# Optimization experiments

Measured on AMD Instinct MI355X. Metric: run time of the kernel, lower is better.

## Reference

```python
import jax, jax.numpy as jnp
import numpy as np

D_MODEL, N_LEVELS, N_HEADS, N_POINTS = 256, 4, 8, 4
SHAPES = [(100, 100), (50, 50), (25, 25), (13, 13)]  # (H, W) per level


def setup_inputs() -> dict:
    key = jax.random.key(0)
    ks = jax.random.split(key, 8)
    N = 2
    C = D_MODEL
    Len_in = sum(h * w for h, w in SHAPES)
    Lq = Len_in  # encoder self-attention
    query = jax.random.normal(ks[0], (N, Lq, C), jnp.float32)
    reference_points = jax.random.uniform(ks[1], (N, Lq, N_LEVELS, 2), dtype=jnp.float32)
    input_flatten = jax.random.normal(ks[2], (N, Len_in, C), jnp.float32)
    input_spatial_shapes = np.array(SHAPES, dtype=np.int64)
    areas = input_spatial_shapes[:, 0] * input_spatial_shapes[:, 1]
    input_level_start_index = np.concatenate([[0], np.cumsum(areas)[:-1]]).astype(np.int64)
    s = 1.0 / np.sqrt(C)
    Wv = jax.random.uniform(ks[3], (C, C), jnp.float32, -s, s)
    bv = jnp.zeros((C,), jnp.float32)
    # sampling_offsets: small random weight + the module's grid bias init
    Woff = jax.random.normal(ks[4], (N_HEADS * N_LEVELS * N_POINTS * 2, C), jnp.float32) * 0.01
    thetas = jnp.arange(N_HEADS, dtype=jnp.float32) * (2.0 * np.pi / N_HEADS)
    grid = jnp.stack([jnp.cos(thetas), jnp.sin(thetas)], -1)  # (M,2)
    grid = grid / jnp.max(jnp.abs(grid), axis=-1, keepdims=True)
    grid = jnp.tile(grid[:, None, None, :], (1, N_LEVELS, N_POINTS, 1))
    grid = grid * (jnp.arange(N_POINTS, dtype=jnp.float32) + 1.0)[None, None, :, None]
    boff = grid.reshape(-1)
    Wa = jax.random.normal(ks[5], (N_HEADS * N_LEVELS * N_POINTS, C), jnp.float32) * 0.02
    ba = jnp.zeros((N_HEADS * N_LEVELS * N_POINTS,), jnp.float32)
    Wo = jax.random.uniform(ks[6], (C, C), jnp.float32, -s, s)
    bo = jnp.zeros((C,), jnp.float32)
    return {
        'query': query, 'reference_points': reference_points, 'input_flatten': input_flatten,
        'input_spatial_shapes': input_spatial_shapes, 'input_level_start_index': input_level_start_index,
        'Wv': Wv, 'bv': bv, 'Woff': Woff, 'boff': boff, 'Wa': Wa, 'ba': ba, 'Wo': Wo, 'bo': bo,
    }


def _msda_forward(query, reference_points, input_flatten, shapes, starts,
                  Wv, bv, Woff, boff, Wa, ba, Wo, bo):
    N, Lq, C = query.shape
    M, L, P = N_HEADS, N_LEVELS, N_POINTS
    D = C // M
    value = (input_flatten @ Wv.T + bv).reshape(N, -1, M, D)  # (N, Len_in, M, D)
    off = (query @ Woff.T + boff).reshape(N, Lq, M, L, P, 2)
    attn = jax.nn.softmax((query @ Wa.T + ba).reshape(N, Lq, M, L * P), axis=-1)
    attn = attn.reshape(N, Lq, M, L, P)
    # offset_normalizer = (W_l, H_l)
    norm = jnp.asarray(shapes[:, ::-1].copy(), jnp.float32)  # (L, 2)
    loc = reference_points[:, :, None, :, None, :] + off / norm[None, None, None, :, None, :]
    grids = 2.0 * loc - 1.0  # (N, Lq, M, L, P, 2), grid_sample convention
    out = jnp.zeros((N, Lq, M, D), query.dtype)
    for l in range(L):
        H, W = int(shapes[l, 0]), int(shapes[l, 1])
        s0 = int(starts[l])
        v = value[:, s0:s0 + H * W]  # (N, H*W, M, D)
        # align_corners=False unnormalization
        gx = ((grids[:, :, :, l, :, 0] + 1.0) * W - 1.0) / 2.0  # (N, Lq, M, P)
        gy = ((grids[:, :, :, l, :, 1] + 1.0) * H - 1.0) / 2.0
        x0 = jnp.floor(gx); y0 = jnp.floor(gy)
        fx = gx - x0;       fy = gy - y0
        x0i = x0.astype(jnp.int32); y0i = y0.astype(jnp.int32)

        def gather(iy, ix):
            valid = (iy >= 0) & (iy < H) & (ix >= 0) & (ix < W)
            lin = jnp.clip(iy, 0, H - 1) * W + jnp.clip(ix, 0, W - 1)  # (N, Lq, M, P)
            lin2 = lin.transpose(0, 1, 3, 2).reshape(N, Lq * P, M)
            g = jnp.take_along_axis(v, lin2[..., None], axis=1)  # (N, Lq*P, M, D)
            g = g.reshape(N, Lq, P, M, D).transpose(0, 1, 3, 2, 4)  # (N, Lq, M, P, D)
            return g * valid[..., None]  # zero padding outside

        s00 = gather(y0i, x0i)
        s01 = gather(y0i, x0i + 1)
        s10 = gather(y0i + 1, x0i)
        s11 = gather(y0i + 1, x0i + 1)
        sampled = (s00 * ((1 - fy) * (1 - fx))[..., None] + s01 * ((1 - fy) * fx)[..., None]
                   + s10 * (fy * (1 - fx))[..., None] + s11 * (fy * fx)[..., None])
        out = out + jnp.einsum('nqmp,nqmpd->nqmd', attn[:, :, :, l], sampled)
    out = out.reshape(N, Lq, C)
    return out @ Wo.T + bo


def reference(query, reference_points, input_flatten, input_spatial_shapes, input_level_start_index,
              Wv, bv, Woff, boff, Wa, ba, Wo, bo):
    shapes = np.asarray(input_spatial_shapes)
    starts = np.asarray(input_level_start_index)
    return _msda_forward(query, reference_points, input_flatten, shapes, starts,
                         Wv, bv, Woff, boff, Wa, ba, Wo, bo)
```

## Files before the change

kernel.cpp:

```cpp
#include <hip/hip_runtime.h>
#include <math.h>

#define NB   2
#define LQ   13294
#define NROWS (NB*LQ)
#define CDIM 256
#define HSLICES (NROWS + 1)
#define HS32 ((size_t)HSLICES * 32)

typedef unsigned short u16;
typedef unsigned int   u32;
typedef short bf16x8 __attribute__((ext_vector_type(8)));
typedef float f32x4  __attribute__((ext_vector_type(4)));
typedef float f32x2  __attribute__((ext_vector_type(2)));

struct alignas(8) U16x4 { u16 x, y, z, w; };

__device__ __forceinline__ u16 f2bf(float f) {
    u32 u = __builtin_bit_cast(u32, f);
    u += 0x7FFFu + ((u >> 16) & 1u);
    return (u16)(u >> 16);
}

__device__ __forceinline__ void gload_lds16(const void* g, void* l) {
    __builtin_amdgcn_global_load_lds(
        (__attribute__((address_space(1))) void*)g,
        (__attribute__((address_space(3))) void*)l, 16, 0, 0);
}

__device__ __forceinline__ f32x2 bfpair(u32 u) {
    union { u32 w[2]; f32x2 v; } x;
    x.w[0] = u << 16;
    x.w[1] = u & 0xFFFF0000u;
    return x.v;
}

__global__ __launch_bounds__(256)
void prep_all(const float4* __restrict__ query, const float4* __restrict__ inflat,
              const float* __restrict__ Wv, const float* __restrict__ Woff,
              const float* __restrict__ Wa, const float* __restrict__ Wo,
              u16* __restrict__ qb, u16* __restrict__ ib,
              u16* __restrict__ wb) {
    const int b = blockIdx.x;
    const int t = threadIdx.x;
    if (b < 6647) {
        int i = b * 256 + t;
        float4 v = query[i];
        U16x4 o{f2bf(v.x), f2bf(v.y), f2bf(v.z), f2bf(v.w)};
        *(U16x4*)&qb[(size_t)i * 4] = o;
    } else if (b < 13294) {
        int i = (b - 6647) * 256 + t;
        float4 v = inflat[i];
        U16x4 o{f2bf(v.x), f2bf(v.y), f2bf(v.z), f2bf(v.w)};
        *(U16x4*)&ib[(size_t)i * 4] = o;
    } else {
        int i = (b - 13294) * 256 + t;
        float v;
        if      (i <  65536) v = Wv[i];
        else if (i < 131072) v = Woff[i - 65536];
        else if (i < 163840) v = Wa[i - 131072];
        else                 v = Wo[i - 163840];
        wb[i] = f2bf(v);
    }
}

__device__ __forceinline__ void gemm_core64(
    const u16* __restrict__ A, const u16* __restrict__ Bw, int M, int row0,
    u16* As, u16* Bs, f32x4 (&acc)[2][4]) {
    const int tid  = threadIdx.x;
    const int lane = tid & 63;
    const int wave = tid >> 6;
    const int ln16 = lane & 15;
    const int kq   = lane >> 4;
    const int wr   = (wave >> 1) * 32;
    const int wc   = (wave & 1) * 64;

    #pragma unroll
    for (int kt = 0; kt < 4; ++kt) {
        const int k0 = kt * 64;
        #pragma unroll
        for (int it = 0; it < 2; ++it) {
            int chunk = it * 256 + tid;
            int row = chunk >> 3, ch = chunk & 7;
            int chs = (ch ^ (row & 7)) * 8;
            int gra = min(row0 + row, M - 1);
            gload_lds16(A + (size_t)gra * 256 + k0 + chs, As + chunk * 8);
        }
        #pragma unroll
        for (int it = 0; it < 4; ++it) {
            int cb = it * 256 + tid;
            int row = cb >> 3, ch = cb & 7;
            int chs = (ch ^ (row & 7)) * 8;
            gload_lds16(Bw + (size_t)row * 256 + k0 + chs, Bs + cb * 8);
        }
        __syncthreads();
        #pragma unroll
        for (int kf = 0; kf < 2; ++kf) {
            const int ck = kf * 4 + kq;
            bf16x8 a[2], b[4];
            #pragma unroll
            for (int i = 0; i < 2; ++i) {
                int r = wr + i * 16 + ln16;
                a[i] = *(const bf16x8*)&As[r * 64 + ((ck ^ (r & 7)) * 8)];
            }
            #pragma unroll
            for (int j = 0; j < 4; ++j) {
                int c = wc + j * 16 + ln16;
                b[j] = *(const bf16x8*)&Bs[c * 64 + ((ck ^ (c & 7)) * 8)];
            }
            #pragma unroll
            for (int i = 0; i < 2; ++i)
                #pragma unroll
                for (int j = 0; j < 4; ++j)
                    acc[i][j] = __builtin_amdgcn_mfma_f32_16x16x32_bf16(
                        a[i], b[j], acc[i][j], 0, 0, 0);
        }
        __syncthreads();
    }
}

__global__ __launch_bounds__(256, 4)
void gemm_front(const u16* __restrict__ qb, const u16* __restrict__ ib,
                const u16* __restrict__ wb, const float* __restrict__ bv,
                const float* __restrict__ boff, const float* __restrict__ ba,
                u16* __restrict__ value, float* __restrict__ offb,
                float* __restrict__ logit, int M) {
    __shared__ u16 Sh[64 * 64 + 128 * 64];
    u16* As = Sh;
    u16* Bs = Sh + 4096;
    const int lid  = blockIdx.x;
    const int xcd  = lid & 7;
    const int idx  = lid >> 3;
    const int rg   = xcd * 52 + idx / 5;
    const int s    = idx % 5;
    const int row0 = rg * 64;
    const u16* A  = (s < 2) ? ib : qb;
    const u16* Bw = wb + (size_t)s * 32768;
    const float* bias = (s == 0) ? bv
                      : (s == 1) ? bv + 128
                      : (s == 2) ? boff
                      : (s == 3) ? boff + 128
                      : ba;

    f32x4 acc[2][4] = {};
    gemm_core64(A, Bw, M, row0, As, Bs, acc);

    const int tid  = threadIdx.x;
    const int lane = tid & 63;
    const int wave = tid >> 6;
    const int ln16 = lane & 15, kq = lane >> 4;
    const int wr = (wave >> 1) * 32, wc = (wave & 1) * 64;

    if (s < 2) {
        #pragma unroll
        for (int j = 0; j < 4; ++j) {
            int cl = wc + j * 16 + ln16;
            float bj = bias[cl];
            #pragma unroll
            for (int i = 0; i < 2; ++i)
                #pragma unroll
                for (int r = 0; r < 4; ++r) {
                    int rl = wr + i * 16 + kq * 4 + r;
                    Sh[rl * 128 + cl] = f2bf(acc[i][j][r] + bj);
                }
        }
        __syncthreads();
        #pragma unroll
        for (int it = 0; it < 4; ++it) {
            int ci = it * 256 + tid;
            int tr = ci >> 4;
            int cc = ci & 15;
            int gr = row0 + tr;
            if (gr < M) {
                int cg = s * 128 + cc * 8;
                u16* dst = value + (size_t)(cg >> 5) * HS32
                                 + (size_t)gr * 32 + (cg & 31);
                *(uint4*)dst = *(const uint4*)&Sh[tr * 128 + cc * 8];
            }
        }
        if (s == 0 && rg == 0) {
            value[(size_t)(tid >> 5) * HS32 + (size_t)NROWS * 32 + (tid & 31)] = 0;
        }
    } else {
        #pragma unroll
        for (int j = 0; j < 4; ++j) {
            int lc = wc + j * 16 + ln16;
            float bj = bias[lc];
            #pragma unroll
            for (int i = 0; i < 2; ++i) {
                #pragma unroll
                for (int r = 0; r < 4; ++r) {
                    int gr = row0 + wr + i * 16 + kq * 4 + r;
                    if (gr < M) {
                        float o = acc[i][j][r] + bj;
                        if (s < 4)
                            offb[(size_t)gr * 256 + (s - 2) * 128 + lc] = o;
                        else
                            logit[(size_t)gr * 128 + lc] = o;
                    }
                }
            }
        }
    }
}

__global__ __launch_bounds__(256, 4)
void gemm_out(const u16* __restrict__ A, const u16* __restrict__ Bw0,
              const float* __restrict__ bias, float* __restrict__ C, int M) {
    __shared__ u16 Sh[64 * 64 + 128 * 64];
    u16* As = Sh;
    u16* Bs = Sh + 4096;
    const int lid  = blockIdx.x;
    const int xcd  = lid & 7;
    const int idx  = lid >> 3;
    const int rg   = xcd * 52 + idx / 2;
    const int s    = idx % 2;
    const int row0 = rg * 64;
    const u16* Bw = Bw0 + (size_t)s * 32768;

    f32x4 acc[2][4] = {};
    gemm_core64(A, Bw, M, row0, As, Bs, acc);

    const int lane = threadIdx.x & 63;
    const int wave = threadIdx.x >> 6;
    const int ln16 = lane & 15, kq = lane >> 4;
    const int wr = (wave >> 1) * 32, wc = (wave & 1) * 64;
    #pragma unroll
    for (int j = 0; j < 4; ++j) {
        int gc = s * 128 + wc + j * 16 + ln16;
        float bj = bias[gc];
        #pragma unroll
        for (int i = 0; i < 2; ++i) {
            #pragma unroll
            for (int r = 0; r < 4; ++r) {
                int gr = row0 + wr + i * 16 + kq * 4 + r;
                if (gr < M) C[(size_t)gr * 256 + gc] = acc[i][j][r] + bj;
            }
        }
    }
}

__global__ __launch_bounds__(256, 4)
void msda_sample(const u16* __restrict__ value,
                 const float* __restrict__ refpts,
                 const float* __restrict__ off,
                 const float* __restrict__ logits,
                 u16* __restrict__ tmp) {
    __shared__ float sAw[4][8][16];
    __shared__ int   sLin[4][8][17][2];
    __shared__ float sW[4][8][17][4];

    const int t  = threadIdx.x;
    const int qb = blockIdx.x * 4;

    if (t < 32) {
        const int qi = t >> 3, m = t & 7;
        const float* lg = logits + (size_t)(qb + qi) * 128 + m * 16;
        float e[16];
        float mx = -1e30f;
        #pragma unroll
        for (int i = 0; i < 16; ++i) { e[i] = lg[i]; mx = fmaxf(mx, e[i]); }
        float s = 0.f;
        #pragma unroll
        for (int i = 0; i < 16; ++i) { e[i] = __expf(e[i] - mx); s += e[i]; }
        const float inv = 1.f / s;
        #pragma unroll
        for (int i = 0; i < 16; ++i) sAw[qi][m][i] = e[i] * inv;
    }
    __syncthreads();

    #pragma unroll
    for (int j2 = 0; j2 < 2; ++j2) {
        const int job = t + j2 * 256;
        const int qi = job >> 7;
        const int m  = (job >> 4) & 7;
        const int p  = job & 15;
        const int l  = p >> 2, pp = p & 3;
        const int q  = qb + qi;
        const int n  = (q >= LQ) ? 1 : 0;

        const int W = (l == 0) ? 100 : (l == 1) ? 50 : (l == 2) ? 25 : 13;
        const int H = W;
        const int st = (l == 0) ? 0 : (l == 1) ? 10000 : (l == 2) ? 12500 : 13125;
        const float invW = (l == 0) ? 0.01f : (l == 1) ? 0.02f
                         : (l == 2) ? 0.04f : (1.f / 13.f);

        const float rx = refpts[(size_t)q * 8 + l * 2 + 0];
        const float ry = refpts[(size_t)q * 8 + l * 2 + 1];
        const float ox = off[(size_t)q * 256 + m * 32 + (l * 4 + pp) * 2 + 0];
        const float oy = off[(size_t)q * 256 + m * 32 + (l * 4 + pp) * 2 + 1];

        const float locx = rx + ox * invW;
        const float locy = ry + oy * invW;
        const float grx = 2.f * locx - 1.f;
        const float gry = 2.f * locy - 1.f;
        const float gx = ((grx + 1.f) * (float)W - 1.f) * 0.5f;
        const float gy = ((gry + 1.f) * (float)H - 1.f) * 0.5f;
        const float x0f = floorf(gx), y0f = floorf(gy);
        const float fx = gx - x0f, fy = gy - y0f;
        const int x0 = (int)x0f, y0 = (int)y0f;
        const int x1 = x0 + 1, y1 = y0 + 1;

        const int cx0 = min(max(x0, 0), W - 1);
        const int cy0 = min(max(y0, 0), H - 1);
        const int cy1 = min(max(y1, 0), H - 1);
        const bool vx0 = (x0 >= 0) & (x0 < W);
        const bool vx1 = (x1 >= 0) & (x1 < W);
        const bool vy0 = (y0 >= 0) & (y0 < H);
        const bool vy1 = (y1 >= 0) & (y1 < H);

        const float aw = sAw[qi][m][p];
        const int base = n * LQ + st;
        const float w00 = (vy0 & vx0) ? aw * (1.f - fy) * (1.f - fx) : 0.f;
        const float w01 = (vy0 & vx1) ? aw * (1.f - fy) * fx         : 0.f;
        const float w10 = (vy1 & vx0) ? aw * fy * (1.f - fx)         : 0.f;
        const float w11 = (vy1 & vx1) ? aw * fy * fx                 : 0.f;
        const bool fold = (x0 < 0);
        sLin[qi][m][p][0] = base + cy0 * W + cx0;
        sLin[qi][m][p][1] = base + cy1 * W + cx0;
        sW[qi][m][p][0] = fold ? w01 : w00;
        sW[qi][m][p][1] = fold ? 0.f : w01;
        sW[qi][m][p][2] = fold ? w11 : w10;
        sW[qi][m][p][3] = fold ? 0.f : w11;
    }
    __syncthreads();

    const int qi = t >> 6;
    const int m  = (t >> 3) & 7;
    const int e  = t & 7;
    const int xh = e >> 2;
    const int c4 = e & 3;
    const int q  = qb + qi;
    const char* vb = (const char*)value + (size_t)m * (HS32 * 2);
    const u32 eoff = (u32)e * 16u;

    f32x2 a2[4] = {{0.f, 0.f}, {0.f, 0.f}, {0.f, 0.f}, {0.f, 0.f}};

    int2   rbA = *(const int2*)  &sLin[qi][m][0][0];
    float4 w4A = *(const float4*)&sW  [qi][m][0][0];
    uint4  rA0 = *(const uint4*)(vb + ((u32)rbA.x * 64u + eoff));
    uint4  rA1 = *(const uint4*)(vb + ((u32)rbA.y * 64u + eoff));

    #pragma unroll
    for (int p = 0; p < 16; ++p) {
        int2   rbB; float4 w4B; uint4 rB0, rB1;
        if (p < 15) {
            rbB = *(const int2*)  &sLin[qi][m][p + 1][0];
            w4B = *(const float4*)&sW  [qi][m][p + 1][0];
            rB0 = *(const uint4*)(vb + ((u32)rbB.x * 64u + eoff));
            rB1 = *(const uint4*)(vb + ((u32)rbB.y * 64u + eoff));
        } else {
            rbB = rbA; w4B = w4A; rB0 = rA0; rB1 = rA1;
        }
        const float wa  = xh ? w4A.y : w4A.x;
        const float wb_ = xh ? w4A.w : w4A.z;
        f32x2 wa2 = {wa, wa};
        f32x2 wb2 = {wb_, wb_};
        a2[0] += wa2 * bfpair(rA0.x); a2[1] += wa2 * bfpair(rA0.y);
        a2[2] += wa2 * bfpair(rA0.z); a2[3] += wa2 * bfpair(rA0.w);
        a2[0] += wb2 * bfpair(rA1.x); a2[1] += wb2 * bfpair(rA1.y);
        a2[2] += wb2 * bfpair(rA1.z); a2[3] += wb2 * bfpair(rA1.w);
        rbA = rbB; w4A = w4B; rA0 = rB0; rA1 = rB1;
    }
    #pragma unroll
    for (int k = 0; k < 4; ++k) {
        a2[k].x += __shfl_xor(a2[k].x, 4);
        a2[k].y += __shfl_xor(a2[k].y, 4);
    }
    if (xh == 0) {
        uint4 o;
        o.x = (u32)f2bf(a2[0].x) | ((u32)f2bf(a2[0].y) << 16);
        o.y = (u32)f2bf(a2[1].x) | ((u32)f2bf(a2[1].y) << 16);
        o.z = (u32)f2bf(a2[2].x) | ((u32)f2bf(a2[2].y) << 16);
        o.w = (u32)f2bf(a2[3].x) | ((u32)f2bf(a2[3].y) << 16);
        *(uint4*)((char*)tmp + ((u32)q * 512u + (u32)m * 64u + (u32)c4 * 16u)) = o;
    }
}

extern "C" void kernel_launch(void* const* d_in, const int* in_sizes, int n_in,
                              void* d_out, int out_size, void* d_ws, size_t ws_size,
                              hipStream_t stream) {
    const float* query  = (const float*)d_in[0];
    const float* refpts = (const float*)d_in[1];
    const float* inflat = (const float*)d_in[2];
    const float* Wv   = (const float*)d_in[5];
    const float* bv   = (const float*)d_in[6];
    const float* Woff = (const float*)d_in[7];
    const float* boff = (const float*)d_in[8];
    const float* Wa   = (const float*)d_in[9];
    const float* ba   = (const float*)d_in[10];
    const float* Wo   = (const float*)d_in[11];
    const float* bo   = (const float*)d_in[12];
    float* out = (float*)d_out;

    char* ws = (char*)d_ws;
    constexpr size_t SZ16  = (size_t)NROWS * 256 * 2;
    constexpr size_t SZVAL = ((size_t)HSLICES * 512 + 4095) & ~(size_t)4095;
    constexpr size_t SZ32  = (size_t)NROWS * 256 * 4;
    constexpr size_t SZL   = (size_t)NROWS * 128 * 4;
    u16*   qb    = (u16*)(ws);
    u16*   ib    = (u16*)(ws + SZ16);
    u16*   value = (u16*)(ws + 2 * SZ16);
    float* offb  = (float*)(ws + 2 * SZ16 + SZVAL);
    float* logit = (float*)(ws + 2 * SZ16 + SZVAL + SZ32);
    u16*   wb    = (u16*)(ws + 2 * SZ16 + SZVAL + SZ32 + SZL);
    u16*   tmp   = qb;

    hipLaunchKernelGGL(prep_all, dim3(14190), dim3(256), 0, stream,
                       (const float4*)query, (const float4*)inflat,
                       Wv, Woff, Wa, Wo, qb, ib, wb);

    gemm_front<<<dim3(2080), dim3(256), 0, stream>>>(
        qb, ib, wb, bv, boff, ba, value, offb, logit, NROWS);

    hipLaunchKernelGGL(msda_sample, dim3(NROWS / 4), dim3(256), 0, stream,
                       value, refpts, offb, logit, tmp);

    gemm_out<<<dim3(832), dim3(256), 0, stream>>>(
        tmp, wb + 163840, bo, out, NROWS);
}
```

Before: 199.7 us.

## Load GEMM MFMA operands directly from global memory, bypassing LDS staging

Replaces the LDS-staged GEMM core (global_load_lds with XOR swizzle and block barriers) with a version where each wave loads its bf16x8 MFMA fragments straight from global memory. This removes the barriers and LDS traffic, and gemm_out no longer needs shared memory, so more blocks may fit per CU. In exchange, operand tiles that several waves share are fetched redundantly through the caches. The 16-byte loads per lane along K are only partly coalesced, and the occupancy hint in launch_bounds is dropped.

```diff
diff --git a/kernel.cpp b/kernel.cpp
--- a/kernel.cpp
+++ b/kernel.cpp
@@ -20,12 +20,6 @@
     u32 u = __builtin_bit_cast(u32, f);
     u += 0x7FFFu + ((u >> 16) & 1u);
     return (u16)(u >> 16);
-}
-
-__device__ __forceinline__ void gload_lds16(const void* g, void* l) {
-    __builtin_amdgcn_global_load_lds(
-        (__attribute__((address_space(1))) void*)g,
-        (__attribute__((address_space(3))) void*)l, 16, 0, 0);
 }
 
 __device__ __forceinline__ f32x2 bfpair(u32 u) {
@@ -64,70 +58,52 @@
     }
 }
 
-__device__ __forceinline__ void gemm_core64(
+__device__ __forceinline__ void gemm_core_direct(
     const u16* __restrict__ A, const u16* __restrict__ Bw, int M, int row0,
-    u16* As, u16* Bs, f32x4 (&acc)[2][4]) {
-    const int tid  = threadIdx.x;
-    const int lane = tid & 63;
-    const int wave = tid >> 6;
+    f32x4 (&acc)[2][4]) {
+    const int lane = threadIdx.x & 63;
+    const int wave = threadIdx.x >> 6;
     const int ln16 = lane & 15;
     const int kq   = lane >> 4;
     const int wr   = (wave >> 1) * 32;
     const int wc   = (wave & 1) * 64;
 
-    #pragma unroll
-    for (int kt = 0; kt < 4; ++kt) {
-        const int k0 = kt * 64;
-        #pragma unroll
-        for (int it = 0; it < 2; ++it) {
-            int chunk = it * 256 + tid;
-            int row = chunk >> 3, ch = chunk & 7;
-            int chs = (ch ^ (row & 7)) * 8;
-            int gra = min(row0 + row, M - 1);
-            gload_lds16(A + (size_t)gra * 256 + k0 + chs, As + chunk * 8);
-        }
-        #pragma unroll
-        for (int it = 0; it < 4; ++it) {
-            int cb = it * 256 + tid;
-            int row = cb >> 3, ch = cb & 7;
-            int chs = (ch ^ (row & 7)) * 8;
-            gload_lds16(Bw + (size_t)row * 256 + k0 + chs, Bs + cb * 8);
-        }
-        __syncthreads();
-        #pragma unroll
-        for (int kf = 0; kf < 2; ++kf) {
-            const int ck = kf * 4 + kq;
-            bf16x8 a[2], b[4];
-            #pragma unroll
-            for (int i = 0; i < 2; ++i) {
-                int r = wr + i * 16 + ln16;
-                a[i] = *(const bf16x8*)&As[r * 64 + ((ck ^ (r & 7)) * 8)];
-            }
-            #pragma unroll
-            for (int j = 0; j < 4; ++j) {
-                int c = wc + j * 16 + ln16;
-                b[j] = *(const bf16x8*)&Bs[c * 64 + ((ck ^ (c & 7)) * 8)];
-            }
-            #pragma unroll
-            for (int i = 0; i < 2; ++i)
-                #pragma unroll
-                for (int j = 0; j < 4; ++j)
-                    acc[i][j] = __builtin_amdgcn_mfma_f32_16x16x32_bf16(
-                        a[i], b[j], acc[i][j], 0, 0, 0);
-        }
-        __syncthreads();
-    }
-}
-
-__global__ __launch_bounds__(256, 4)
+    const int ra0 = min(row0 + wr      + ln16, M - 1);
+    const int ra1 = min(row0 + wr + 16 + ln16, M - 1);
+    const u16* pa0 = A  + (size_t)ra0 * 256 + kq * 8;
+    const u16* pa1 = A  + (size_t)ra1 * 256 + kq * 8;
+    const u16* pb0 = Bw + (size_t)(wc      + ln16) * 256 + kq * 8;
+    const u16* pb1 = Bw + (size_t)(wc + 16 + ln16) * 256 + kq * 8;
+    const u16* pb2 = Bw + (size_t)(wc + 32 + ln16) * 256 + kq * 8;
+    const u16* pb3 = Bw + (size_t)(wc + 48 + ln16) * 256 + kq * 8;
+
+    #pragma unroll
+    for (int kf = 0; kf < 8; ++kf) {
+        const int ko = kf * 32;
+        bf16x8 a0 = *(const bf16x8*)(pa0 + ko);
+        bf16x8 a1 = *(const bf16x8*)(pa1 + ko);
+        bf16x8 b0 = *(const bf16x8*)(pb0 + ko);
+        bf16x8 b1 = *(const bf16x8*)(pb1 + ko);
+        bf16x8 b2 = *(const bf16x8*)(pb2 + ko);
+        bf16x8 b3 = *(const bf16x8*)(pb3 + ko);
+        acc[0][0] = __builtin_amdgcn_mfma_f32_16x16x32_bf16(a0, b0, acc[0][0], 0, 0, 0);
+        acc[0][1] = __builtin_amdgcn_mfma_f32_16x16x32_bf16(a0, b1, acc[0][1], 0, 0, 0);
+        acc[0][2] = __builtin_amdgcn_mfma_f32_16x16x32_bf16(a0, b2, acc[0][2], 0, 0, 0);
+        acc[0][3] = __builtin_amdgcn_mfma_f32_16x16x32_bf16(a0, b3, acc[0][3], 0, 0, 0);
+        acc[1][0] = __builtin_amdgcn_mfma_f32_16x16x32_bf16(a1, b0, acc[1][0], 0, 0, 0);
+        acc[1][1] = __builtin_amdgcn_mfma_f32_16x16x32_bf16(a1, b1, acc[1][1], 0, 0, 0);
+        acc[1][2] = __builtin_amdgcn_mfma_f32_16x16x32_bf16(a1, b2, acc[1][2], 0, 0, 0);
+        acc[1][3] = __builtin_amdgcn_mfma_f32_16x16x32_bf16(a1, b3, acc[1][3], 0, 0, 0);
+    }
+}
+
+__global__ __launch_bounds__(256)
 void gemm_front(const u16* __restrict__ qb, const u16* __restrict__ ib,
                 const u16* __restrict__ wb, const float* __restrict__ bv,
                 const float* __restrict__ boff, const float* __restrict__ ba,
                 u16* __restrict__ value, float* __restrict__ offb,
                 float* __restrict__ logit, int M) {
-    __shared__ u16 Sh[64 * 64 + 128 * 64];
-    u16* As = Sh;
-    u16* Bs = Sh + 4096;
+    __shared__ u16 Sh[64 * 128];
     const int lid  = blockIdx.x;
     const int xcd  = lid & 7;
     const int idx  = lid >> 3;
@@ -143,7 +119,7 @@
                       : ba;
 
     f32x4 acc[2][4] = {};
-    gemm_core64(A, Bw, M, row0, As, Bs, acc);
+    gemm_core_direct(A, Bw, M, row0, acc);
 
     const int tid  = threadIdx.x;
     const int lane = tid & 63;
@@ -204,12 +180,9 @@
     }
 }
 
-__global__ __launch_bounds__(256, 4)
+__global__ __launch_bounds__(256)
 void gemm_out(const u16* __restrict__ A, const u16* __restrict__ Bw0,
               const float* __restrict__ bias, float* __restrict__ C, int M) {
-    __shared__ u16 Sh[64 * 64 + 128 * 64];
-    u16* As = Sh;
-    u16* Bs = Sh + 4096;
     const int lid  = blockIdx.x;
     const int xcd  = lid & 7;
     const int idx  = lid >> 3;
@@ -219,7 +192,7 @@
     const u16* Bw = Bw0 + (size_t)s * 32768;
 
     f32x4 acc[2][4] = {};
-    gemm_core64(A, Bw, M, row0, As, Bs, acc);
+    gemm_core_direct(A, Bw, M, row0, acc);
 
     const int lane = threadIdx.x & 63;
     const int wave = threadIdx.x >> 6;
```

Result: slower. 255.1 us (+27.7%).

## Fuse fp32-to-bf16 activation conversion into front GEMM A-tile loads

Applied to the files above, without the earlier changes.

Removes the separate pass that converted query and input_flatten to bf16. The front GEMM now loads fp32 A tiles straight into LDS with a swizzle and converts them to bf16 in registers with v_cvt_pk_bf16_f32 before the MFMA. Only the small weight conversion remains as its own kernel. This saves a full read and write of both activations, but each A tile now moves twice as many bytes and takes twice the LDS, and the four weight-shard blocks per row group each re-read the fp32 rows.

```diff
diff --git a/kernel.cpp b/kernel.cpp
--- a/kernel.cpp
+++ b/kernel.cpp
@@ -22,6 +22,12 @@
     return (u16)(u >> 16);
 }
 
+__device__ __forceinline__ u32 cvtpk(float a, float b) {
+    u32 d;
+    asm("v_cvt_pk_bf16_f32 %0, %1, %2" : "=v"(d) : "v"(a), "v"(b));
+    return d;
+}
+
 __device__ __forceinline__ void gload_lds16(const void* g, void* l) {
     __builtin_amdgcn_global_load_lds(
         (__attribute__((address_space(1))) void*)g,
@@ -36,32 +42,16 @@
 }
 
 __global__ __launch_bounds__(256)
-void prep_all(const float4* __restrict__ query, const float4* __restrict__ inflat,
-              const float* __restrict__ Wv, const float* __restrict__ Woff,
-              const float* __restrict__ Wa, const float* __restrict__ Wo,
-              u16* __restrict__ qb, u16* __restrict__ ib,
-              u16* __restrict__ wb) {
-    const int b = blockIdx.x;
-    const int t = threadIdx.x;
-    if (b < 6647) {
-        int i = b * 256 + t;
-        float4 v = query[i];
-        U16x4 o{f2bf(v.x), f2bf(v.y), f2bf(v.z), f2bf(v.w)};
-        *(U16x4*)&qb[(size_t)i * 4] = o;
-    } else if (b < 13294) {
-        int i = (b - 6647) * 256 + t;
-        float4 v = inflat[i];
-        U16x4 o{f2bf(v.x), f2bf(v.y), f2bf(v.z), f2bf(v.w)};
-        *(U16x4*)&ib[(size_t)i * 4] = o;
-    } else {
-        int i = (b - 13294) * 256 + t;
-        float v;
-        if      (i <  65536) v = Wv[i];
-        else if (i < 131072) v = Woff[i - 65536];
-        else if (i < 163840) v = Wa[i - 131072];
-        else                 v = Wo[i - 163840];
-        wb[i] = f2bf(v);
-    }
+void prep_w(const float* __restrict__ Wv, const float* __restrict__ Woff,
+            const float* __restrict__ Wa, const float* __restrict__ Wo,
+            u16* __restrict__ wb) {
+    int i = blockIdx.x * 256 + threadIdx.x;
+    float v;
+    if      (i <  65536) v = Wv[i];
+    else if (i < 131072) v = Woff[i - 65536];
+    else if (i < 163840) v = Wa[i - 131072];
+    else                 v = Wo[i - 163840];
+    wb[i] = f2bf(v);
 }
 
 __device__ __forceinline__ void gemm_core64(
@@ -119,23 +109,84 @@
     }
 }
 
+__device__ __forceinline__ void gemm_core64_f32A(
+    const float* __restrict__ A, const u16* __restrict__ Bw, int M, int row0,
+    float* Asf, u16* Bs, f32x4 (&acc)[2][4]) {
+    const int tid  = threadIdx.x;
+    const int lane = tid & 63;
+    const int wave = tid >> 6;
+    const int ln16 = lane & 15;
+    const int kq   = lane >> 4;
+    const int wr   = (wave >> 1) * 32;
+    const int wc   = (wave & 1) * 64;
+
+    #pragma unroll
+    for (int kt = 0; kt < 4; ++kt) {
+        const int k0 = kt * 64;
+        #pragma unroll
+        for (int it = 0; it < 4; ++it) {
+            int chunk = it * 256 + tid;
+            int row = chunk >> 4, ch = chunk & 15;
+            int gra = min(row0 + row, M - 1);
+            gload_lds16(A + (size_t)gra * 256 + k0 + ((ch ^ (row & 15)) << 2),
+                        Asf + chunk * 4);
+        }
+        #pragma unroll
+        for (int it = 0; it < 4; ++it) {
+            int cb = it * 256 + tid;
+            int row = cb >> 3, ch = cb & 7;
+            gload_lds16(Bw + (size_t)row * 256 + k0 + ((ch ^ (row & 7)) * 8),
+                        Bs + cb * 8);
+        }
+        __syncthreads();
+        #pragma unroll
+        for (int kf = 0; kf < 2; ++kf) {
+            const int ck = kf * 4 + kq;
+            bf16x8 a[2], b[4];
+            #pragma unroll
+            for (int i = 0; i < 2; ++i) {
+                int r = wr + i * 16 + ln16;
+                int c0 = (kf * 8 + 2 * kq)     ^ (r & 15);
+                int c1 = (kf * 8 + 2 * kq + 1) ^ (r & 15);
+                float4 lo = *(const float4*)&Asf[r * 64 + c0 * 4];
+                float4 hi = *(const float4*)&Asf[r * 64 + c1 * 4];
+                union { u32 u[4]; bf16x8 v; } ua;
+                ua.u[0] = cvtpk(lo.x, lo.y); ua.u[1] = cvtpk(lo.z, lo.w);
+                ua.u[2] = cvtpk(hi.x, hi.y); ua.u[3] = cvtpk(hi.z, hi.w);
+                a[i] = ua.v;
+            }
+            #pragma unroll
+            for (int j = 0; j < 4; ++j) {
+                int c = wc + j * 16 + ln16;
+                b[j] = *(const bf16x8*)&Bs[c * 64 + ((ck ^ (c & 7)) * 8)];
+            }
+            #pragma unroll
+            for (int i = 0; i < 2; ++i)
+                #pragma unroll
+                for (int j = 0; j < 4; ++j)
+                    acc[i][j] = __builtin_amdgcn_mfma_f32_16x16x32_bf16(
+                        a[i], b[j], acc[i][j], 0, 0, 0);
+        }
+        __syncthreads();
+    }
+}
+
 __global__ __launch_bounds__(256, 4)
-void gemm_front(const u16* __restrict__ qb, const u16* __restrict__ ib,
+void gemm_front(const float* __restrict__ query, const float* __restrict__ inflat,
                 const u16* __restrict__ wb, const float* __restrict__ bv,
                 const float* __restrict__ boff, const float* __restrict__ ba,
                 u16* __restrict__ value, float* __restrict__ offb,
                 float* __restrict__ logit, int M) {
-    __shared__ u16 Sh[64 * 64 + 128 * 64];
-    u16* As = Sh;
-    u16* Bs = Sh + 4096;
+    __shared__ float Asf[64 * 64];
+    __shared__ u16   Bs[128 * 64];
     const int lid  = blockIdx.x;
     const int xcd  = lid & 7;
     const int idx  = lid >> 3;
     const int rg   = xcd * 52 + idx / 5;
     const int s    = idx % 5;
     const int row0 = rg * 64;
-    const u16* A  = (s < 2) ? ib : qb;
-    const u16* Bw = wb + (size_t)s * 32768;
+    const float* A = (s < 2) ? inflat : query;
+    const u16* Bw  = wb + (size_t)s * 32768;
     const float* bias = (s == 0) ? bv
                       : (s == 1) ? bv + 128
                       : (s == 2) ? boff
@@ -143,7 +194,7 @@
                       : ba;
 
     f32x4 acc[2][4] = {};
-    gemm_core64(A, Bw, M, row0, As, Bs, acc);
+    gemm_core64_f32A(A, Bw, M, row0, Asf, Bs, acc);
 
     const int tid  = threadIdx.x;
     const int lane = tid & 63;
@@ -152,6 +203,7 @@
     const int wr = (wave >> 1) * 32, wc = (wave & 1) * 64;
 
     if (s < 2) {
+        u16* Sh = (u16*)Asf;
         #pragma unroll
         for (int j = 0; j < 4; ++j) {
             int cl = wc + j * 16 + ln16;
@@ -397,21 +449,17 @@
     constexpr size_t SZ16  = (size_t)NROWS * 256 * 2;
     constexpr size_t SZVAL = ((size_t)HSLICES * 512 + 4095) & ~(size_t)4095;
     constexpr size_t SZ32  = (size_t)NROWS * 256 * 4;
-    constexpr size_t SZL   = (size_t)NROWS * 128 * 4;
-    u16*   qb    = (u16*)(ws);
-    u16*   ib    = (u16*)(ws + SZ16);
-    u16*   value = (u16*)(ws + 2 * SZ16);
-    float* offb  = (float*)(ws + 2 * SZ16 + SZVAL);
-    float* logit = (float*)(ws + 2 * SZ16 + SZVAL + SZ32);
-    u16*   wb    = (u16*)(ws + 2 * SZ16 + SZVAL + SZ32 + SZL);
-    u16*   tmp   = qb;
-
-    hipLaunchKernelGGL(prep_all, dim3(14190), dim3(256), 0, stream,
-                       (const float4*)query, (const float4*)inflat,
-                       Wv, Woff, Wa, Wo, qb, ib, wb);
+    u16*   tmp   = (u16*)(ws);
+    u16*   value = (u16*)(ws + SZ16);
+    float* offb  = (float*)(ws + SZ16 + SZVAL);
+    float* logit = (float*)(ws + SZ16 + SZVAL + SZ32);
+    u16*   wb    = (u16*)(ws + SZ16 + SZVAL + SZ32 + (size_t)NROWS * 128 * 4);
+
+    hipLaunchKernelGGL(prep_w, dim3(896), dim3(256), 0, stream,
+                       Wv, Woff, Wa, Wo, wb);
 
     gemm_front<<<dim3(2080), dim3(256), 0, stream>>>(
-        qb, ib, wb, bv, boff, ba, value, offb, logit, NROWS);
+        query, inflat, wb, bv, boff, ba, value, offb, logit, NROWS);
 
     hipLaunchKernelGGL(msda_sample, dim3(NROWS / 4), dim3(256), 0, stream,
                        value, refpts, offb, logit, tmp);
```

After: 207.6 us. +3.9%, slower.

## Fuse output projection GEMM into the deformable sampling kernel

Applied to the files above, without the earlier changes.

Drops the separate gemm_out kernel. Each sampling block now stages its 4 sampled bf16 query rows in shared memory and multiplies them by Wo with MFMA, adding the bias and writing the final fp32 output directly. This removes one kernel launch and the global write and re-read of the intermediate tmp buffer. In exchange, every block streams the whole 256x256 bf16 Wo matrix from cache for only 4 rows. The 16-row MFMA tiles are also only a quarter used, so cache traffic and matrix-unit waste rise sharply.

```diff
diff --git a/kernel.cpp b/kernel.cpp
--- a/kernel.cpp
+++ b/kernel.cpp
@@ -205,50 +205,17 @@
 }
 
 __global__ __launch_bounds__(256, 4)
-void gemm_out(const u16* __restrict__ A, const u16* __restrict__ Bw0,
-              const float* __restrict__ bias, float* __restrict__ C, int M) {
-    __shared__ u16 Sh[64 * 64 + 128 * 64];
-    u16* As = Sh;
-    u16* Bs = Sh + 4096;
-    const int lid  = blockIdx.x;
-    const int xcd  = lid & 7;
-    const int idx  = lid >> 3;
-    const int rg   = xcd * 52 + idx / 2;
-    const int s    = idx % 2;
-    const int row0 = rg * 64;
-    const u16* Bw = Bw0 + (size_t)s * 32768;
-
-    f32x4 acc[2][4] = {};
-    gemm_core64(A, Bw, M, row0, As, Bs, acc);
-
-    const int lane = threadIdx.x & 63;
-    const int wave = threadIdx.x >> 6;
-    const int ln16 = lane & 15, kq = lane >> 4;
-    const int wr = (wave >> 1) * 32, wc = (wave & 1) * 64;
-    #pragma unroll
-    for (int j = 0; j < 4; ++j) {
-        int gc = s * 128 + wc + j * 16 + ln16;
-        float bj = bias[gc];
-        #pragma unroll
-        for (int i = 0; i < 2; ++i) {
-            #pragma unroll
-            for (int r = 0; r < 4; ++r) {
-                int gr = row0 + wr + i * 16 + kq * 4 + r;
-                if (gr < M) C[(size_t)gr * 256 + gc] = acc[i][j][r] + bj;
-            }
-        }
-    }
-}
-
-__global__ __launch_bounds__(256, 4)
 void msda_sample(const u16* __restrict__ value,
                  const float* __restrict__ refpts,
                  const float* __restrict__ off,
                  const float* __restrict__ logits,
-                 u16* __restrict__ tmp) {
+                 const u16* __restrict__ wo,
+                 const float* __restrict__ bo,
+                 float* __restrict__ out) {
     __shared__ float sAw[4][8][16];
     __shared__ int   sLin[4][8][17][2];
     __shared__ float sW[4][8][17][4];
+    __shared__ u16   sTmp[16 * 264];
 
     const int t  = threadIdx.x;
     const int qb = blockIdx.x * 4;
@@ -325,55 +292,94 @@
     }
     __syncthreads();
 
-    const int qi = t >> 6;
-    const int m  = (t >> 3) & 7;
-    const int e  = t & 7;
-    const int xh = e >> 2;
-    const int c4 = e & 3;
-    const int q  = qb + qi;
-    const char* vb = (const char*)value + (size_t)m * (HS32 * 2);
-    const u32 eoff = (u32)e * 16u;
-
-    f32x2 a2[4] = {{0.f, 0.f}, {0.f, 0.f}, {0.f, 0.f}, {0.f, 0.f}};
-
-    int2   rbA = *(const int2*)  &sLin[qi][m][0][0];
-    float4 w4A = *(const float4*)&sW  [qi][m][0][0];
-    uint4  rA0 = *(const uint4*)(vb + ((u32)rbA.x * 64u + eoff));
-    uint4  rA1 = *(const uint4*)(vb + ((u32)rbA.y * 64u + eoff));
-
-    #pragma unroll
-    for (int p = 0; p < 16; ++p) {
-        int2   rbB; float4 w4B; uint4 rB0, rB1;
-        if (p < 15) {
-            rbB = *(const int2*)  &sLin[qi][m][p + 1][0];
-            w4B = *(const float4*)&sW  [qi][m][p + 1][0];
-            rB0 = *(const uint4*)(vb + ((u32)rbB.x * 64u + eoff));
-            rB1 = *(const uint4*)(vb + ((u32)rbB.y * 64u + eoff));
-        } else {
-            rbB = rbA; w4B = w4A; rB0 = rA0; rB1 = rA1;
-        }
-        const float wa  = xh ? w4A.y : w4A.x;
-        const float wb_ = xh ? w4A.w : w4A.z;
-        f32x2 wa2 = {wa, wa};
-        f32x2 wb2 = {wb_, wb_};
-        a2[0] += wa2 * bfpair(rA0.x); a2[1] += wa2 * bfpair(rA0.y);
-        a2[2] += wa2 * bfpair(rA0.z); a2[3] += wa2 * bfpair(rA0.w);
-        a2[0] += wb2 * bfpair(rA1.x); a2[1] += wb2 * bfpair(rA1.y);
-        a2[2] += wb2 * bfpair(rA1.z); a2[3] += wb2 * bfpair(rA1.w);
-        rbA = rbB; w4A = w4B; rA0 = rB0; rA1 = rB1;
-    }
-    #pragma unroll
-    for (int k = 0; k < 4; ++k) {
-        a2[k].x += __shfl_xor(a2[k].x, 4);
-        a2[k].y += __shfl_xor(a2[k].y, 4);
-    }
-    if (xh == 0) {
-        uint4 o;
-        o.x = (u32)f2bf(a2[0].x) | ((u32)f2bf(a2[0].y) << 16);
-        o.y = (u32)f2bf(a2[1].x) | ((u32)f2bf(a2[1].y) << 16);
-        o.z = (u32)f2bf(a2[2].x) | ((u32)f2bf(a2[2].y) << 16);
-        o.w = (u32)f2bf(a2[3].x) | ((u32)f2bf(a2[3].y) << 16);
-        *(uint4*)((char*)tmp + ((u32)q * 512u + (u32)m * 64u + (u32)c4 * 16u)) = o;
+    {
+        const int qi = t >> 6;
+        const int m  = (t >> 3) & 7;
+        const int e  = t & 7;
+        const int xh = e >> 2;
+        const int c4 = e & 3;
+        const char* vb = (const char*)value + (size_t)m * (HS32 * 2);
+        const u32 eoff = (u32)e * 16u;
+
+        f32x2 a2[4] = {{0.f, 0.f}, {0.f, 0.f}, {0.f, 0.f}, {0.f, 0.f}};
+
+        int2   rbA = *(const int2*)  &sLin[qi][m][0][0];
+        float4 w4A = *(const float4*)&sW  [qi][m][0][0];
+        uint4  rA0 = *(const uint4*)(vb + ((u32)rbA.x * 64u + eoff));
+        uint4  rA1 = *(const uint4*)(vb + ((u32)rbA.y * 64u + eoff));
+
+        #pragma unroll
+        for (int p = 0; p < 16; ++p) {
+            int2   rbB; float4 w4B; uint4 rB0, rB1;
+            if (p < 15) {
+                rbB = *(const int2*)  &sLin[qi][m][p + 1][0];
+                w4B = *(const float4*)&sW  [qi][m][p + 1][0];
+                rB0 = *(const uint4*)(vb + ((u32)rbB.x * 64u + eoff));
+                rB1 = *(const uint4*)(vb + ((u32)rbB.y * 64u + eoff));
+            } else {
+                rbB = rbA; w4B = w4A; rB0 = rA0; rB1 = rA1;
+            }
+            const float wa  = xh ? w4A.y : w4A.x;
+            const float wb_ = xh ? w4A.w : w4A.z;
+            f32x2 wa2 = {wa, wa};
+            f32x2 wb2 = {wb_, wb_};
+            a2[0] += wa2 * bfpair(rA0.x); a2[1] += wa2 * bfpair(rA0.y);
+            a2[2] += wa2 * bfpair(rA0.z); a2[3] += wa2 * bfpair(rA0.w);
+            a2[0] += wb2 * bfpair(rA1.x); a2[1] += wb2 * bfpair(rA1.y);
+            a2[2] += wb2 * bfpair(rA1.z); a2[3] += wb2 * bfpair(rA1.w);
+            rbA = rbB; w4A = w4B; rA0 = rB0; rA1 = rB1;
+        }
+        #pragma unroll
+        for (int k = 0; k < 4; ++k) {
+            a2[k].x += __shfl_xor(a2[k].x, 4);
+            a2[k].y += __shfl_xor(a2[k].y, 4);
+        }
+        if (xh == 0) {
+            uint4 o;
+            o.x = (u32)f2bf(a2[0].x) | ((u32)f2bf(a2[0].y) << 16);
+            o.y = (u32)f2bf(a2[1].x) | ((u32)f2bf(a2[1].y) << 16);
+            o.z = (u32)f2bf(a2[2].x) | ((u32)f2bf(a2[2].y) << 16);
+            o.w = (u32)f2bf(a2[3].x) | ((u32)f2bf(a2[3].y) << 16);
+            *(uint4*)&sTmp[qi * 264 + m * 32 + c4 * 8] = o;
+        }
+    }
+    __syncthreads();
+
+    {
+        const int lane = t & 63;
+        const int wv   = t >> 6;
+        const int ln16 = lane & 15;
+        const int kq   = lane >> 4;
+        const int wc   = wv * 64;
+        const u16* wo0 = wo + (size_t)(wc      + ln16) * 256 + kq * 8;
+        const u16* wo1 = wo0 + 16 * 256;
+        const u16* wo2 = wo0 + 32 * 256;
+        const u16* wo3 = wo0 + 48 * 256;
+        const u16* ap  = &sTmp[ln16 * 264 + kq * 8];
+        f32x4 ac0 = {}, ac1 = {}, ac2 = {}, ac3 = {};
+        #pragma unroll
+        for (int ks = 0; ks < 8; ++ks) {
+            bf16x8 av = *(const bf16x8*)(ap  + ks * 32);
+            bf16x8 b0 = *(const bf16x8*)(wo0 + ks * 32);
+            bf16x8 b1 = *(const bf16x8*)(wo1 + ks * 32);
+            bf16x8 b2 = *(const bf16x8*)(wo2 + ks * 32);
+            bf16x8 b3 = *(const bf16x8*)(wo3 + ks * 32);
+            ac0 = __builtin_amdgcn_mfma_f32_16x16x32_bf16(av, b0, ac0, 0, 0, 0);
+            ac1 = __builtin_amdgcn_mfma_f32_16x16x32_bf16(av, b1, ac1, 0, 0, 0);
+            ac2 = __builtin_amdgcn_mfma_f32_16x16x32_bf16(av, b2, ac2, 0, 0, 0);
+            ac3 = __builtin_amdgcn_mfma_f32_16x16x32_bf16(av, b3, ac3, 0, 0, 0);
+        }
+        if (kq == 0) {
+            #pragma unroll
+            for (int j = 0; j < 4; ++j) {
+                int gc = wc + j * 16 + ln16;
+                float bj = bo[gc];
+                f32x4 a = (j == 0) ? ac0 : (j == 1) ? ac1 : (j == 2) ? ac2 : ac3;
+                #pragma unroll
+                for (int r = 0; r < 4; ++r)
+                    out[(size_t)(qb + r) * 256 + gc] = a[r] + bj;
+            }
+        }
     }
 }
 
@@ -404,7 +410,6 @@
     float* offb  = (float*)(ws + 2 * SZ16 + SZVAL);
     float* logit = (float*)(ws + 2 * SZ16 + SZVAL + SZ32);
     u16*   wb    = (u16*)(ws + 2 * SZ16 + SZVAL + SZ32 + SZL);
-    u16*   tmp   = qb;
 
     hipLaunchKernelGGL(prep_all, dim3(14190), dim3(256), 0, stream,
                        (const float4*)query, (const float4*)inflat,
@@ -414,8 +419,5 @@
         qb, ib, wb, bv, boff, ba, value, offb, logit, NROWS);
 
     hipLaunchKernelGGL(msda_sample, dim3(NROWS / 4), dim3(256), 0, stream,
-                       value, refpts, offb, logit, tmp);
-
-    gemm_out<<<dim3(832), dim3(256), 0, stream>>>(
-        tmp, wb + 163840, bo, out, NROWS);
-}
+                       value, refpts, offb, logit, wb + 163840, bo, out);
+}
```

After: 273.6 us. 1.37x slower.
